# Optimization experiments

Hardware: AMD Instinct MI355X
Metric: run time of the kernel (lower is better)

Reference implementation:

```python
import jax, jax.numpy as jnp
import numpy as np

B, N, D_IN, D_OUT, H = 2, 2048, 1024, 1024, 16
HEAD_DIM = D_OUT // H


def setup_inputs() -> dict:
    key = jax.random.key(0)
    ks = jax.random.split(key, 8)
    s = 0.02
    return {
        "x": jax.random.normal(ks[0], (B, N, D_IN), dtype=jnp.float32),
        "Wq": jax.random.normal(ks[1], (D_IN, D_OUT), dtype=jnp.float32) * s,
        "Wk": jax.random.normal(ks[2], (D_IN, D_OUT), dtype=jnp.float32) * s,
        "Wv": jax.random.normal(ks[3], (D_IN, D_OUT), dtype=jnp.float32) * s,
        "Wo": jax.random.normal(ks[4], (D_OUT, D_OUT), dtype=jnp.float32) * s,
        "bo": jnp.zeros((D_OUT,), dtype=jnp.float32),
        "w": jax.random.uniform(ks[5], (H,), dtype=jnp.float32),
        "v": jax.random.uniform(ks[6], (H,), dtype=jnp.float32),
    }


def reference(x, Wq, Wk, Wv, Wo, bo, w, v):
    b, n, _ = x.shape
    h = w.shape[0]
    hd = Wq.shape[1] // h

    # QKV projections -> [b, h, n, hd]
    def proj(W):
        return (x @ W).reshape(b, n, h, hd).transpose(0, 2, 1, 3)

    q, k, val = proj(Wq), proj(Wk), proj(Wv)

    # relative-distance decay R_hat: [h, n, n]
    pos = jnp.arange(n)
    R = jnp.abs(pos[:, None] - pos[None, :]).astype(x.dtype)  # [n, n]
    wv = w[:, None, None]
    vv = v[:, None, None]
    R_hat = (1.0 + jnp.exp(vv)) / (1.0 + jnp.exp(vv - wv * R))  # [h, n, n]

    # ReLU(QK^T) * R_hat, causal mask, scaled softmax
    scores = jax.nn.relu(jnp.einsum("bhqd,bhkd->bhqk", q, k)) * R_hat[None]
    causal = jnp.triu(jnp.ones((n, n), dtype=bool), k=1)
    scores = jnp.where(causal[None, None], -jnp.inf, scores)
    attn = jax.nn.softmax(scores / np.sqrt(hd).astype(x.dtype), axis=-1)

    ctx = jnp.einsum("bhqk,bhkd->bhqd", attn, val)
    ctx = ctx.transpose(0, 2, 1, 3).reshape(b, n, h * hd)
    return ctx @ Wo + bo
```

## Files before the change

### kernel.cpp

```cpp
#include <hip/hip_runtime.h>

typedef unsigned short u16;
typedef unsigned int u32;
typedef __attribute__((ext_vector_type(8))) short bf16x8;
typedef __attribute__((ext_vector_type(4))) float f32x4;

__device__ __forceinline__ u16 f2bf(float f) {
    u32 u = __float_as_uint(f);
    u += 0x7fffu + ((u >> 16) & 1u);
    return (u16)(u >> 16);
}

__device__ __forceinline__ u32 cvtpk(float lo, float hi) {
    u32 r;
    asm("v_cvt_pk_bf16_f32 %0, %1, %2" : "=v"(r) : "v"(lo), "v"(hi));
    return r;
}

#define GL2LDS(gp, lp)                                                                 \
    __builtin_amdgcn_global_load_lds((const __attribute__((address_space(1))) u32*)(const void*)(gp), \
                                     (__attribute__((address_space(3))) u32*)(void*)(lp), 16, 0, 0)

#define SBAR                                                                           \
    do {                                                                               \
        __builtin_amdgcn_sched_barrier(0);                                             \
        __builtin_amdgcn_s_barrier();                                                  \
        __builtin_amdgcn_sched_barrier(0);                                             \
    } while (0)
#define WAITV(N)                                                                       \
    do {                                                                               \
        asm volatile("s_waitcnt vmcnt(" #N ")" ::: "memory");                          \
        __builtin_amdgcn_sched_barrier(0);                                             \
    } while (0)

__global__ __launch_bounds__(256) void prep_kernel(const float* __restrict__ x,
                                                   const float* __restrict__ Wq,
                                                   const float* __restrict__ Wk,
                                                   const float* __restrict__ Wv,
                                                   const float* __restrict__ Wo,
                                                   const float* __restrict__ wp,
                                                   const float* __restrict__ vp,
                                                   u16* __restrict__ xb,
                                                   u16* __restrict__ Wcat,
                                                   u16* __restrict__ Wot,
                                                   float* __restrict__ tab,
                                                   u32* __restrict__ counter) {
    __shared__ float tl[32][33];
    const int bid = blockIdx.x, t = threadIdx.x;
    if (bid < 4096) {
        const int i = bid * 256 + t;
        float4 val = ((const float4*)x)[i];
        uint2 o;
        o.x = cvtpk(val.x, val.y);
        o.y = cvtpk(val.z, val.w);
        ((uint2*)xb)[i] = o;
    } else if (bid < 8192) {
        const int tid = bid - 4096;
        const int zi = tid >> 10, rem = tid & 1023;
        const int kt = (rem >> 5) * 32, nt = (rem & 31) * 32;
        const float* src = (zi == 0) ? Wq : (zi == 1) ? Wk : (zi == 2) ? Wv : Wo;
        u16* dst = (zi < 3) ? (Wcat + zi * 1048576) : Wot;
        const int tx = t & 31, ty = t >> 5;
#pragma unroll
        for (int j = 0; j < 4; ++j)
            tl[ty + j * 8][tx] = src[(kt + ty + j * 8) * 1024 + nt + tx];
        __syncthreads();
#pragma unroll
        for (int j = 0; j < 4; ++j)
            dst[(nt + ty + j * 8) * 1024 + kt + tx] = f2bf(tl[tx][ty + j * 8]);
    } else {
        const int i = (bid - 8192) * 256 + t;
        if (i == 0) counter[0] = 0u;
        const int h = i >> 11, d = i & 2047;
        const float vv = vp[h], ww = wp[h];
        tab[i] = (1.f + expf(vv)) / (1.f + expf(vv - ww * (float)d)) *
                 (0.125f * 1.44269504088896340736f);
    }
}

template <int MODE, int BN>
__global__ __launch_bounds__(256, 3) void gemm128(const u16* __restrict__ A,
                                                  const u16* __restrict__ Bt,
                                                  float* __restrict__ C,
                                                  const float* __restrict__ bias,
                                                  u16* __restrict__ Cb,
                                                  u16* __restrict__ Vt,
                                                  int M, int N, int K) {
    constexpr int NBW = BN / 32;
    __shared__ __align__(16) u16 As[8192];
    __shared__ __align__(16) u16 Bs[BN * 64];
    const int t = threadIdx.x, lane = t & 63, wv = t >> 6;
    const int l15 = lane & 15, quad = lane >> 4;
    const int m0 = blockIdx.y << 7, n0 = blockIdx.x * BN;
    const int wm = (wv & 1) << 6, wn = (wv >> 1) * (BN / 2);

    f32x4 acc[4][NBW];
#pragma unroll
    for (int i = 0; i < 4; ++i)
#pragma unroll
        for (int j = 0; j < NBW; ++j) acc[i][j] = (f32x4){0.f, 0.f, 0.f, 0.f};

    const int lrow = lane >> 3, lchunk = lane & 7;
    for (int k0 = 0; k0 < K; k0 += 64) {
#pragma unroll
        for (int c = 0; c < 4; ++c) {
            const int r0 = wv * 32 + c * 8;
            const int row = r0 + lrow;
            const int g = lchunk ^ (row & 7);
            GL2LDS(A + (size_t)(m0 + row) * K + k0 + g * 8, &As[r0 * 64]);
        }
#pragma unroll
        for (int c = 0; c < BN / 32; ++c) {
            const int r0 = wv * (BN / 4) + c * 8;
            const int row = r0 + lrow;
            const int g = lchunk ^ (row & 7);
            GL2LDS(Bt + (size_t)(n0 + row) * K + k0 + g * 8, &Bs[r0 * 64]);
        }
        __syncthreads();
#pragma unroll
        for (int ks = 0; ks < 2; ++ks) {
            const int p = ((ks << 2) | quad) ^ (l15 & 7);
            bf16x8 af[4], bfr[NBW];
#pragma unroll
            for (int i = 0; i < 4; ++i)
                af[i] = *(const bf16x8*)&As[(wm + i * 16 + l15) * 64 + p * 8];
#pragma unroll
            for (int j = 0; j < NBW; ++j)
                bfr[j] = *(const bf16x8*)&Bs[(wn + j * 16 + l15) * 64 + p * 8];
#pragma unroll
            for (int mb = 0; mb < 4; ++mb)
#pragma unroll
                for (int nb = 0; nb < NBW; ++nb)
                    acc[mb][nb] = __builtin_amdgcn_mfma_f32_16x16x32_bf16(af[mb], bfr[nb],
                                                                          acc[mb][nb], 0, 0, 0);
        }
        __syncthreads();
    }
    const int rb = m0 + wm + (quad << 2);
    const int cbase = n0 + wn + l15;
#pragma unroll
    for (int mb = 0; mb < 4; ++mb)
#pragma unroll
        for (int nb = 0; nb < NBW; ++nb) {
            const int col = cbase + nb * 16;
            if (MODE == 0) {
#pragma unroll
                for (int r = 0; r < 4; ++r) {
                    const int row = rb + mb * 16 + r;
                    C[(size_t)row * N + col] = acc[mb][nb][r] + bias[col];
                }
            } else if (col < 2048) {
#pragma unroll
                for (int r = 0; r < 4; ++r) {
                    const int row = rb + mb * 16 + r;
                    Cb[(size_t)row * 2048 + col] = f2bf(acc[mb][nb][r]);
                }
            } else {
                const int pos = (((mb >> 1) * 4 + quad) << 3) + ((mb & 1) << 2);
                uint2 o;
                o.x = cvtpk(acc[mb][nb][0], acc[mb][nb][1]);
                o.y = cvtpk(acc[mb][nb][2], acc[mb][nb][3]);
                *(uint2*)(Vt + (size_t)(col - 2048) * 4096 + (m0 + wm) + pos) = o;
            }
        }
}

__global__ __launch_bounds__(256, 3) void attn_kernel(const u16* __restrict__ qkb,
                                                      const u16* __restrict__ vtb,
                                                      const float* __restrict__ rtab,
                                                      u16* __restrict__ ctxb,
                                                      u32* __restrict__ counter) {
    __shared__ __align__(16) u16 Kt[3][4096];
    __shared__ __align__(16) u16 Vt2[2][4096];
    __shared__ __align__(16) float rall[2048];
    __shared__ int jobS;

    const int t = threadIdx.x, lane = t & 63, wv = t >> 6;
    const int l15 = lane & 15, quad = lane >> 4;
    const int lrow = lane >> 3, lchunk = lane & 7;
    const int half0 = (wv & 1) * 32;

    for (;;) {
        if (t == 0) jobS = (int)atomicAdd(counter, 1u);
        __syncthreads();
        const int job = jobS;
        if (job >= 1024) break;
        const int qt = 31 - (job >> 5);
        const int bh = job & 31;
        const int b = bh >> 4, h = bh & 15;
        const int q0 = qt << 6;

        {
            const float4* src = (const float4*)(rtab + (h << 11));
            const int nf = (q0 + 64) >> 2;
            for (int i = t; i < nf; i += 256) ((float4*)rall)[i] = src[i];
        }

        bf16x8 qb[2];
        {
            const u16* qrow = qkb + (size_t)(b * 2048 + q0 + (wv << 4) + l15) * 2048 +
                              (h << 6) + quad * 8;
            qb[0] = *(const bf16x8*)(qrow);
            qb[1] = *(const bf16x8*)(qrow + 32);
        }

        auto stage_k = [&](int ktile, int kb) {
#pragma unroll
            for (int c = 0; c < 4; ++c) {
                const int r0 = half0 + c * 8;
                const int row = r0 + lrow;
                const int g = lchunk ^ (row & 7);
                GL2LDS(qkb + (size_t)(b * 2048 + (ktile << 6) + row) * 2048 + 1024 +
                           (h << 6) + g * 8,
                       &Kt[kb][r0 * 64]);
            }
        };
        auto stage_v = [&](int ktile, int vb) {
#pragma unroll
            for (int c = 0; c < 4; ++c) {
                const int r0 = half0 + c * 8;
                const int row = r0 + lrow;
                const int g = lchunk ^ (row & 7);
                GL2LDS(vtb + (size_t)((h << 6) + row) * 4096 + b * 2048 + (ktile << 6) +
                           g * 8,
                       &Vt2[vb][r0 * 64]);
            }
        };

        f32x4 cacc[4];
#pragma unroll
        for (int i = 0; i < 4; ++i) cacc[i] = (f32x4){0.f, 0.f, 0.f, 0.f};
        f32x4 lacc4 = (f32x4){0.f, 0.f, 0.f, 0.f};

        if (wv < 2) {
            stage_k(0, 0);
            if (qt >= 1) stage_k(1, 1);
        } else {
            stage_v(0, 0);
        }
        asm volatile("s_waitcnt lgkmcnt(0)" ::: "memory");
        __builtin_amdgcn_sched_barrier(0);

        for (int kt = 0; kt <= qt; ++kt) {
            const int kb = kt % 3, vb = kt & 1;
            if (wv < 2) {
                if (kt < qt) WAITV(4);
                else         WAITV(0);
            }
            SBAR;
            if (wv < 2) {
                if (kt + 2 <= qt) stage_k(kt + 2, (kt + 2) % 3);
            } else {
                if (kt + 1 <= qt) stage_v(kt + 1, (kt + 1) & 1);
            }

            f32x4 sacc[4];
#pragma unroll
            for (int i = 0; i < 4; ++i) sacc[i] = (f32x4){0.f, 0.f, 0.f, 0.f};
            __builtin_amdgcn_s_setprio(1);
#pragma unroll
            for (int ks = 0; ks < 2; ++ks) {
                const int p = ((ks << 2) | quad) ^ (l15 & 7);
#pragma unroll
                for (int mb = 0; mb < 4; ++mb) {
                    bf16x8 ka = *(const bf16x8*)&Kt[kb][(mb * 16 + l15) * 64 + p * 8];
                    sacc[mb] = __builtin_amdgcn_mfma_f32_16x16x32_bf16(ka, qb[ks],
                                                                       sacc[mb], 0, 0, 0);
                }
            }
            __builtin_amdgcn_s_setprio(0);

            const int D0 = q0 - (kt << 6) + (wv << 4) + l15;
            u32 pk[4][2];
            if (kt < qt) {
#pragma unroll
                for (int mb = 0; mb < 4; ++mb) {
                    float pe[4];
#pragma unroll
                    for (int r = 0; r < 4; ++r) {
                        const int dist = D0 - (mb * 16 + (quad << 2) + r);
                        pe[r] = exp2f(fmaxf(sacc[mb][r], 0.f) * rall[dist]);
                        lacc4[r] += pe[r];
                    }
                    pk[mb][0] = cvtpk(pe[0], pe[1]);
                    pk[mb][1] = cvtpk(pe[2], pe[3]);
                }
            } else {
#pragma unroll
                for (int mb = 0; mb < 4; ++mb) {
                    float pe[4];
#pragma unroll
                    for (int r = 0; r < 4; ++r) {
                        const int dist = D0 - (mb * 16 + (quad << 2) + r);
                        const int di = dist < 0 ? 0 : dist;
                        float p0 = exp2f(fmaxf(sacc[mb][r], 0.f) * rall[di]);
                        pe[r] = (dist < 0) ? 0.f : p0;
                        lacc4[r] += pe[r];
                    }
                    pk[mb][0] = cvtpk(pe[0], pe[1]);
                    pk[mb][1] = cvtpk(pe[2], pe[3]);
                }
            }

            if (wv >= 2) {
                if (kt < qt) WAITV(4);
                else         WAITV(0);
            }
            SBAR;

            __builtin_amdgcn_s_setprio(1);
#pragma unroll
            for (int ks = 0; ks < 2; ++ks) {
                int4 pv = {(int)pk[2 * ks][0], (int)pk[2 * ks][1],
                           (int)pk[2 * ks + 1][0], (int)pk[2 * ks + 1][1]};
                bf16x8 pb = *(bf16x8*)&pv;
                const int g = (4 * ks + quad) ^ (l15 & 7);
#pragma unroll
                for (int db = 0; db < 4; ++db) {
                    bf16x8 vf = *(const bf16x8*)&Vt2[vb][(db * 16 + l15) * 64 + g * 8];
                    cacc[db] = __builtin_amdgcn_mfma_f32_16x16x32_bf16(vf, pb,
                                                                       cacc[db], 0, 0, 0);
                }
            }
            __builtin_amdgcn_s_setprio(0);
        }

        float lt = (lacc4[0] + lacc4[1]) + (lacc4[2] + lacc4[3]);
        lt += __shfl_xor(lt, 16, 64);
        lt += __shfl_xor(lt, 32, 64);
        const float inv = 1.f / lt;
        u16* op = ctxb + (size_t)(b * 2048 + q0 + (wv << 4) + l15) * 1024 +
                  (h << 6) + (quad << 2);
#pragma unroll
        for (int db = 0; db < 4; ++db) {
            uint2 o;
            o.x = cvtpk(cacc[db][0] * inv, cacc[db][1] * inv);
            o.y = cvtpk(cacc[db][2] * inv, cacc[db][3] * inv);
            *(uint2*)(op + db * 16) = o;
        }
    }
}

extern "C" void kernel_launch(void* const* d_in, const int* in_sizes, int n_in,
                              void* d_out, int out_size, void* d_ws, size_t ws_size,
                              hipStream_t stream) {
    const float* x  = (const float*)d_in[0];
    const float* Wq = (const float*)d_in[1];
    const float* Wk = (const float*)d_in[2];
    const float* Wv = (const float*)d_in[3];
    const float* Wo = (const float*)d_in[4];
    const float* bo = (const float*)d_in[5];
    const float* w  = (const float*)d_in[6];
    const float* v  = (const float*)d_in[7];
    float* out = (float*)d_out;

    char* w8 = (char*)d_ws;
    u16*  xb   = (u16*)(w8);
    u16*  Wcat = (u16*)(w8 + (8u << 20));
    u16*  Wot  = (u16*)(w8 + (14u << 20));
    u16*  qkb  = (u16*)(w8 + (16u << 20));
    u16*  vtb  = (u16*)(w8 + (32u << 20));
    u16*  ctxb = (u16*)(w8 + (40u << 20));
    float* rtab = (float*)(w8 + (48u << 20));
    u32*  counter = (u32*)(w8 + (48u << 20) + (1u << 17));

    prep_kernel<<<8320, 256, 0, stream>>>(x, Wq, Wk, Wv, Wo, w, v, xb, Wcat, Wot, rtab,
                                          counter);
    gemm128<1, 128><<<dim3(24, 32), 256, 0, stream>>>(xb, Wcat, nullptr, nullptr, qkb, vtb,
                                                      4096, 3072, 1024);
    attn_kernel<<<768, 256, 0, stream>>>(qkb, vtb, rtab, ctxb, counter);
    gemm128<0, 64><<<dim3(16, 32), 256, 0, stream>>>(ctxb, Wot, out, bo, nullptr, nullptr,
                                                     4096, 1024, 1024);
}
```

Measured before the change: 184.3 us.

## Software-pipeline PV matmul one tile behind QK to drop a barrier per tile

Restructures the attention inner loop so that the P·V MFMA for tile kt-1 runs right after the QK^T MFMA for tile kt, with a single barrier per iteration instead of two. The K buffer ring shrinks from 3 to 2 slots and the V ring grows from 2 to 3 so V stays resident one extra iteration, and the final PV step is issued after the loop. The aim is to remove a block-wide sync per tile and overlap PV matrix work with the exp/softmax VALU work. In exchange, K prefetch depth drops from two tiles ahead to one, which may expose more load latency.

```diff
diff --git a/kernel.cpp b/kernel.cpp
--- a/kernel.cpp
+++ b/kernel.cpp
@@ -170,8 +170,8 @@
                                                       const float* __restrict__ rtab,
                                                       u16* __restrict__ ctxb,
                                                       u32* __restrict__ counter) {
-    __shared__ __align__(16) u16 Kt[3][4096];
-    __shared__ __align__(16) u16 Vt2[2][4096];
+    __shared__ __align__(16) u16 Kt[2][4096];
+    __shared__ __align__(16) u16 Vt2[3][4096];
     __shared__ __align__(16) float rall[2048];
     __shared__ int jobS;
 
@@ -226,32 +226,40 @@
                        &Vt2[vb][r0 * 64]);
             }
         };
+        auto pv_step = [&](const u32 (&pk)[4][2], int vb, f32x4 (&cacc)[4]) {
+#pragma unroll
+            for (int ks = 0; ks < 2; ++ks) {
+                int4 pv = {(int)pk[2 * ks][0], (int)pk[2 * ks][1],
+                           (int)pk[2 * ks + 1][0], (int)pk[2 * ks + 1][1]};
+                bf16x8 pb = *(bf16x8*)&pv;
+                const int g = (4 * ks + quad) ^ (l15 & 7);
+#pragma unroll
+                for (int db = 0; db < 4; ++db) {
+                    bf16x8 vf = *(const bf16x8*)&Vt2[vb][(db * 16 + l15) * 64 + g * 8];
+                    cacc[db] = __builtin_amdgcn_mfma_f32_16x16x32_bf16(vf, pb,
+                                                                       cacc[db], 0, 0, 0);
+                }
+            }
+        };
 
         f32x4 cacc[4];
 #pragma unroll
         for (int i = 0; i < 4; ++i) cacc[i] = (f32x4){0.f, 0.f, 0.f, 0.f};
         f32x4 lacc4 = (f32x4){0.f, 0.f, 0.f, 0.f};
-
-        if (wv < 2) {
-            stage_k(0, 0);
-            if (qt >= 1) stage_k(1, 1);
-        } else {
-            stage_v(0, 0);
-        }
+        u32 pkp[4][2];
+
+        if (wv < 2) stage_k(0, 0);
+        else        stage_v(0, 0);
         asm volatile("s_waitcnt lgkmcnt(0)" ::: "memory");
         __builtin_amdgcn_sched_barrier(0);
 
         for (int kt = 0; kt <= qt; ++kt) {
-            const int kb = kt % 3, vb = kt & 1;
-            if (wv < 2) {
-                if (kt < qt) WAITV(4);
-                else         WAITV(0);
-            }
+            if (wv < 2) WAITV(0);
+            else        WAITV(4);
             SBAR;
-            if (wv < 2) {
-                if (kt + 2 <= qt) stage_k(kt + 2, (kt + 2) % 3);
-            } else {
-                if (kt + 1 <= qt) stage_v(kt + 1, (kt + 1) & 1);
+            if (kt < qt) {
+                if (wv < 2) stage_k(kt + 1, (kt + 1) & 1);
+                else        stage_v(kt + 1, (kt + 1) % 3);
             }
 
             f32x4 sacc[4];
@@ -263,15 +271,15 @@
                 const int p = ((ks << 2) | quad) ^ (l15 & 7);
 #pragma unroll
                 for (int mb = 0; mb < 4; ++mb) {
-                    bf16x8 ka = *(const bf16x8*)&Kt[kb][(mb * 16 + l15) * 64 + p * 8];
+                    bf16x8 ka = *(const bf16x8*)&Kt[kt & 1][(mb * 16 + l15) * 64 + p * 8];
                     sacc[mb] = __builtin_amdgcn_mfma_f32_16x16x32_bf16(ka, qb[ks],
                                                                        sacc[mb], 0, 0, 0);
                 }
             }
+            if (kt > 0) pv_step(pkp, (kt - 1) % 3, cacc);
             __builtin_amdgcn_s_setprio(0);
 
             const int D0 = q0 - (kt << 6) + (wv << 4) + l15;
-            u32 pk[4][2];
             if (kt < qt) {
 #pragma unroll
                 for (int mb = 0; mb < 4; ++mb) {
@@ -282,8 +290,8 @@
                         pe[r] = exp2f(fmaxf(sacc[mb][r], 0.f) * rall[dist]);
                         lacc4[r] += pe[r];
                     }
-                    pk[mb][0] = cvtpk(pe[0], pe[1]);
-                    pk[mb][1] = cvtpk(pe[2], pe[3]);
+                    pkp[mb][0] = cvtpk(pe[0], pe[1]);
+                    pkp[mb][1] = cvtpk(pe[2], pe[3]);
                 }
             } else {
 #pragma unroll
@@ -297,33 +305,17 @@
                         pe[r] = (dist < 0) ? 0.f : p0;
                         lacc4[r] += pe[r];
                     }
-                    pk[mb][0] = cvtpk(pe[0], pe[1]);
-                    pk[mb][1] = cvtpk(pe[2], pe[3]);
-                }
-            }
-
-            if (wv >= 2) {
-                if (kt < qt) WAITV(4);
-                else         WAITV(0);
-            }
-            SBAR;
-
-            __builtin_amdgcn_s_setprio(1);
-#pragma unroll
-            for (int ks = 0; ks < 2; ++ks) {
-                int4 pv = {(int)pk[2 * ks][0], (int)pk[2 * ks][1],
-                           (int)pk[2 * ks + 1][0], (int)pk[2 * ks + 1][1]};
-                bf16x8 pb = *(bf16x8*)&pv;
-                const int g = (4 * ks + quad) ^ (l15 & 7);
-#pragma unroll
-                for (int db = 0; db < 4; ++db) {
-                    bf16x8 vf = *(const bf16x8*)&Vt2[vb][(db * 16 + l15) * 64 + g * 8];
-                    cacc[db] = __builtin_amdgcn_mfma_f32_16x16x32_bf16(vf, pb,
-                                                                       cacc[db], 0, 0, 0);
-                }
-            }
-            __builtin_amdgcn_s_setprio(0);
-        }
+                    pkp[mb][0] = cvtpk(pe[0], pe[1]);
+                    pkp[mb][1] = cvtpk(pe[2], pe[3]);
+                }
+            }
+        }
+
+        WAITV(0);
+        SBAR;
+        __builtin_amdgcn_s_setprio(1);
+        pv_step(pkp, qt % 3, cacc);
+        __builtin_amdgcn_s_setprio(0);
 
         float lt = (lacc4[0] + lacc4[1]) + (lacc4[2] + lacc4[3]);
         lt += __shfl_xor(lt, 16, 64);
```

Result: no change. 186.3 us (+1.1%).

## Replace QKV projection GEMM with 256x256-tile, 512-thread pipelined kernel

Applied to the files above, without the earlier changes.

Adds a dedicated gemm256 kernel for the fused QKV projection. It uses 256x256 output tiles, 8 waves, and 128 KB of dynamic LDS with double-buffered, half-K staged global-to-LDS loads interleaved with MFMA phases. The goal is more operand reuse per block and overlap of loads with matrix math. The risk is that the grid shrinks to 192 blocks, fewer than the CU count, which leaves some CUs idle. The generic gemm128 is simplified to only the output-projection mode.

```diff
diff --git a/kernel.cpp b/kernel.cpp
--- a/kernel.cpp
+++ b/kernel.cpp
@@ -30,6 +30,11 @@
 #define WAITV(N)                                                                       \
     do {                                                                               \
         asm volatile("s_waitcnt vmcnt(" #N ")" ::: "memory");                          \
+        __builtin_amdgcn_sched_barrier(0);                                             \
+    } while (0)
+#define WAITLGKM0                                                                      \
+    do {                                                                               \
+        asm volatile("s_waitcnt lgkmcnt(0)" ::: "memory");                             \
         __builtin_amdgcn_sched_barrier(0);                                             \
     } while (0)
 
@@ -78,13 +83,114 @@
     }
 }
 
+__global__ __launch_bounds__(512, 2) void gemm256(const u16* __restrict__ A,
+                                                  const u16* __restrict__ Bt,
+                                                  u16* __restrict__ Cb,
+                                                  u16* __restrict__ Vt) {
+    extern __shared__ u16 sm[];
+    const int t = threadIdx.x, lane = t & 63, w = t >> 6;
+    const int l15 = lane & 15, quad = lane >> 4;
+    const int wr = w >> 2, wc = w & 3;
+    const int m0 = blockIdx.y << 8, n0 = blockIdx.x << 8;
+    const int srow = lane >> 2, sc = lane & 3;
+
+    f32x4 acc[8][4];
+#pragma unroll
+    for (int i = 0; i < 8; ++i)
+#pragma unroll
+        for (int j = 0; j < 4; ++j) acc[i][j] = (f32x4){0.f, 0.f, 0.f, 0.f};
+
+    auto stage = [&](int O, int kt, int kh) {
+        const u16* src = O ? Bt : A;
+        const int g0 = O ? n0 : m0;
+        const int base = O * 32768 + (kt & 1) * 16384 + kh * 8192;
+        const int k0 = (kt << 6) + (kh << 5);
+#pragma unroll
+        for (int j = 0; j < 2; ++j) {
+            const int row = (w * 2 + j) * 16 + srow;
+            const int g = (sc ^ (row & 3)) << 3;
+            GL2LDS(src + (size_t)(g0 + row) * 1024 + k0 + g,
+                   &sm[base + (w * 2 + j) * 512]);
+        }
+    };
+
+    auto phase = [&](int d, int mh, int kh, auto&& stg, int wmode) {
+        bf16x8 af[4], bf[4];
+        const int ab = d * 16384 + kh * 8192;
+        const int bb = 32768 + d * 16384 + kh * 8192;
+#pragma unroll
+        for (int mm = 0; mm < 4; ++mm) {
+            const int row = wr * 128 + mh * 64 + mm * 16 + l15;
+            af[mm] = *(const bf16x8*)&sm[ab + row * 32 + ((quad ^ (row & 3)) << 3)];
+        }
+#pragma unroll
+        for (int nn = 0; nn < 4; ++nn) {
+            const int row = wc * 64 + nn * 16 + l15;
+            bf[nn] = *(const bf16x8*)&sm[bb + row * 32 + ((quad ^ (row & 3)) << 3)];
+        }
+        stg();
+        SBAR;
+        WAITLGKM0;
+        __builtin_amdgcn_s_setprio(1);
+#pragma unroll
+        for (int mm = 0; mm < 4; ++mm)
+#pragma unroll
+            for (int nn = 0; nn < 4; ++nn)
+                acc[mh * 4 + mm][nn] = __builtin_amdgcn_mfma_f32_16x16x32_bf16(
+                    af[mm], bf[nn], acc[mh * 4 + mm][nn], 0, 0, 0);
+        __builtin_amdgcn_s_setprio(0);
+        if (wmode == 1) WAITV(8);
+        else if (wmode == 2) WAITV(4);
+        else if (wmode == 3) WAITV(0);
+        SBAR;
+    };
+
+    stage(0, 0, 0); stage(1, 0, 0); stage(0, 0, 1); stage(1, 0, 1);
+    stage(0, 1, 0); stage(1, 1, 0);
+    WAITV(8);
+    SBAR;
+
+    for (int i = 0; i < 8; ++i) {
+        const bool nl = (i < 7);
+        phase(0, 0, 0, [&] { stage(0, 2 * i + 1, 1); }, 0);
+        phase(0, 1, 0, [&] { stage(1, 2 * i + 1, 1); }, 1);
+        phase(0, 0, 1, [&] { if (nl) stage(0, 2 * i + 2, 0); }, 0);
+        phase(0, 1, 1, [&] { if (nl) stage(1, 2 * i + 2, 0); }, nl ? 1 : 2);
+        phase(1, 0, 0, [&] { if (nl) stage(0, 2 * i + 2, 1); }, 0);
+        phase(1, 1, 0, [&] { if (nl) stage(1, 2 * i + 2, 1); }, nl ? 1 : 3);
+        phase(1, 0, 1, [&] { if (nl) stage(0, 2 * i + 3, 0); }, 0);
+        phase(1, 1, 1, [&] { if (nl) stage(1, 2 * i + 3, 0); }, nl ? 1 : 0);
+    }
+
+    const int cb0 = n0 + wc * 64;
+#pragma unroll
+    for (int am = 0; am < 8; ++am) {
+#pragma unroll
+        for (int nn = 0; nn < 4; ++nn) {
+            const int col = cb0 + nn * 16 + l15;
+            if (n0 < 2048) {
+                const int row = m0 + wr * 128 + am * 16 + (quad << 2);
+#pragma unroll
+                for (int r = 0; r < 4; ++r)
+                    Cb[(size_t)(row + r) * 2048 + col] = f2bf(acc[am][nn][r]);
+            } else {
+                const int mm = am & 3, mh = am >> 2;
+                const int win = m0 + wr * 128 + mh * 64;
+                const int pos = (((mm >> 1) * 4 + quad) << 3) + ((mm & 1) << 2);
+                uint2 o;
+                o.x = cvtpk(acc[am][nn][0], acc[am][nn][1]);
+                o.y = cvtpk(acc[am][nn][2], acc[am][nn][3]);
+                *(uint2*)(Vt + (size_t)(col - 2048) * 4096 + win + pos) = o;
+            }
+        }
+    }
+}
+
 template <int MODE, int BN>
 __global__ __launch_bounds__(256, 3) void gemm128(const u16* __restrict__ A,
                                                   const u16* __restrict__ Bt,
                                                   float* __restrict__ C,
                                                   const float* __restrict__ bias,
-                                                  u16* __restrict__ Cb,
-                                                  u16* __restrict__ Vt,
                                                   int M, int N, int K) {
     constexpr int NBW = BN / 32;
     __shared__ __align__(16) u16 As[8192];
@@ -143,24 +249,10 @@
 #pragma unroll
         for (int nb = 0; nb < NBW; ++nb) {
             const int col = cbase + nb * 16;
-            if (MODE == 0) {
-#pragma unroll
-                for (int r = 0; r < 4; ++r) {
-                    const int row = rb + mb * 16 + r;
-                    C[(size_t)row * N + col] = acc[mb][nb][r] + bias[col];
-                }
-            } else if (col < 2048) {
-#pragma unroll
-                for (int r = 0; r < 4; ++r) {
-                    const int row = rb + mb * 16 + r;
-                    Cb[(size_t)row * 2048 + col] = f2bf(acc[mb][nb][r]);
-                }
-            } else {
-                const int pos = (((mb >> 1) * 4 + quad) << 3) + ((mb & 1) << 2);
-                uint2 o;
-                o.x = cvtpk(acc[mb][nb][0], acc[mb][nb][1]);
-                o.y = cvtpk(acc[mb][nb][2], acc[mb][nb][3]);
-                *(uint2*)(Vt + (size_t)(col - 2048) * 4096 + (m0 + wm) + pos) = o;
+#pragma unroll
+            for (int r = 0; r < 4; ++r) {
+                const int row = rb + mb * 16 + r;
+                C[(size_t)row * N + col] = acc[mb][nb][r] + bias[col];
             }
         }
 }
@@ -238,8 +330,7 @@
         } else {
             stage_v(0, 0);
         }
-        asm volatile("s_waitcnt lgkmcnt(0)" ::: "memory");
-        __builtin_amdgcn_sched_barrier(0);
+        WAITLGKM0;
 
         for (int kt = 0; kt <= qt; ++kt) {
             const int kb = kt % 3, vb = kt & 1;
@@ -364,11 +455,16 @@
     float* rtab = (float*)(w8 + (48u << 20));
     u32*  counter = (u32*)(w8 + (48u << 20) + (1u << 17));
 
+    static bool attrSet = false;
+    if (!attrSet) {
+        hipFuncSetAttribute(reinterpret_cast<const void*>(gemm256),
+                            hipFuncAttributeMaxDynamicSharedMemorySize, 131072);
+        attrSet = true;
+    }
+
     prep_kernel<<<8320, 256, 0, stream>>>(x, Wq, Wk, Wv, Wo, w, v, xb, Wcat, Wot, rtab,
                                           counter);
-    gemm128<1, 128><<<dim3(24, 32), 256, 0, stream>>>(xb, Wcat, nullptr, nullptr, qkb, vtb,
-                                                      4096, 3072, 1024);
+    gemm256<<<dim3(12, 16), 512, 131072, stream>>>(xb, Wcat, qkb, vtb);
     attn_kernel<<<768, 256, 0, stream>>>(qkb, vtb, rtab, ctxb, counter);
-    gemm128<0, 64><<<dim3(16, 32), 256, 0, stream>>>(ctxb, Wot, out, bo, nullptr, nullptr,
-                                                     4096, 1024, 1024);
-}
+    gemm128<0, 64><<<dim3(16, 32), 256, 0, stream>>>(ctxb, Wot, out, bo, 4096, 1024, 1024);
+}
```

After: 196.3 us. +6.5%, slower.
